# Kernel tuning notes

Hardware: AMD Instinct MI355X
Metric: run time of the kernel (lower is better)

## Reference

```python
import jax, jax.numpy as jnp
import numpy as np

N_NODES = 50000
N_EDGES = 800000
NFEAT = 128
NHID = 64
NLAYER = 3
BN_EPS = 1e-5


def _bn(h, gamma, beta):
    # BatchNorm1d, training-mode batch statistics (biased variance)
    mu = jnp.mean(h, axis=0)
    var = jnp.mean((h - mu) ** 2, axis=0)
    return gamma * (h - mu) * jax.lax.rsqrt(var + BN_EPS) + beta


def setup_inputs() -> dict:
    key = jax.random.key(0)
    ks = jax.random.split(key, 8)
    x = jax.random.normal(ks[0], (N_NODES, NFEAT), dtype=jnp.float32)
    edge_index = jax.random.randint(ks[1], (2, N_EDGES), 0, N_NODES, dtype=jnp.int64)
    # transform: Linear(nfeat, nhid) with bias, then BN
    W_t = jax.random.normal(ks[2], (NFEAT, NHID), dtype=jnp.float32) / np.sqrt(NFEAT)
    b_t = jnp.zeros((NHID,), dtype=jnp.float32)
    g_t = jnp.ones((NHID,), dtype=jnp.float32)
    bb_t = jnp.zeros((NHID,), dtype=jnp.float32)
    # per-layer GIN MLPs (bias=False) and BN affine params, stacked over layers
    W1 = jax.random.normal(ks[3], (NLAYER, NHID, NHID), dtype=jnp.float32) / np.sqrt(NHID)
    W2 = jax.random.normal(ks[4], (NLAYER, NHID, NHID), dtype=jnp.float32) / np.sqrt(NHID)
    gamma = jnp.ones((NLAYER, NHID), dtype=jnp.float32)
    beta = jnp.zeros((NLAYER, NHID), dtype=jnp.float32)
    return {"x": x, "edge_index": edge_index, "W_t": W_t, "b_t": b_t,
            "g_t": g_t, "bb_t": bb_t, "W1": W1, "W2": W2,
            "gamma": gamma, "beta": beta}


def reference(x, edge_index, W_t, b_t, g_t, bb_t, W1, W2, gamma, beta):
    src, dst = edge_index[0], edge_index[1]
    # input transform: Linear + BN
    h = _bn(x @ W_t + b_t, g_t, bb_t)
    for i in range(NLAYER):
        # dropout p=0 -> identity
        # GINConv (eps=0): (1+eps)*h + sum_{j->i} h_j, then 2-layer MLP
        agg = h + jax.ops.segment_sum(h[src], dst, num_segments=N_NODES)
        h = jax.nn.relu(agg @ W1[i]) @ W2[i]
        h = jax.nn.relu(h)
        h = _bn(h, gamma[i], beta[i])
    # per-graph boolean-mask split is a pure partition of rows; return full matrix
    return h
```

## Files before the change

kernel.cpp:

```cpp
#include <hip/hip_runtime.h>

#define NND 50000
#define NED 800000
#define NF  128
#define NH  64
#define BN_EPS 1e-5
#define NCOPY 64
#define SCB  256
#define NSB  ((NND + SCB - 1) / SCB)
#define XNODES (NND / 8)
#define FCH  196

#define WS_HA     0
#define WS_STATS  12800000
#define WS_SSF    (WS_STATS + NCOPY*128*8)
#define WS_DEG    (WS_SSF + 512)
#define WS_OFFS   (WS_DEG + NND*4)
#define WS_CUR    (WS_OFFS + (NND+4)*4)
#define WS_PARTS  (WS_CUR + NND*4)
#define WS_ESRC   (WS_PARTS + 256*4)

__global__ __launch_bounds__(256) void k_deg(const int* __restrict__ dst,
                                             int* __restrict__ deg) {
    int xcd = blockIdx.x & 7;
    int chunk = blockIdx.x >> 3;
    int lo = xcd * XNODES;
    const int4* d4 = (const int4*)dst;
#pragma unroll
    for (int r = 0; r < 4; ++r) {
        int i = chunk * 1024 + r * 256 + threadIdx.x;
        if (i < NED / 4) {
            int4 d = d4[i];
            if ((unsigned)(d.x - lo) < XNODES) atomicAdd(&deg[d.x], 1);
            if ((unsigned)(d.y - lo) < XNODES) atomicAdd(&deg[d.y], 1);
            if ((unsigned)(d.z - lo) < XNODES) atomicAdd(&deg[d.z], 1);
            if ((unsigned)(d.w - lo) < XNODES) atomicAdd(&deg[d.w], 1);
        }
    }
}

__global__ __launch_bounds__(256) void k_fill(const int* __restrict__ src,
                                              const int* __restrict__ dst,
                                              int* __restrict__ cur,
                                              int* __restrict__ esrc) {
    int xcd = blockIdx.x & 7;
    int chunk = blockIdx.x >> 3;
    int lo = xcd * XNODES;
    const int4* d4 = (const int4*)dst;
#pragma unroll
    for (int r = 0; r < 4; ++r) {
        int i = chunk * 1024 + r * 256 + threadIdx.x;
        if (i < NED / 4) {
            int4 d = d4[i];
            int e = i * 4;
            if ((unsigned)(d.x - lo) < XNODES) esrc[atomicAdd(&cur[d.x], 1)] = src[e];
            if ((unsigned)(d.y - lo) < XNODES) esrc[atomicAdd(&cur[d.y], 1)] = src[e + 1];
            if ((unsigned)(d.z - lo) < XNODES) esrc[atomicAdd(&cur[d.z], 1)] = src[e + 2];
            if ((unsigned)(d.w - lo) < XNODES) esrc[atomicAdd(&cur[d.w], 1)] = src[e + 3];
        }
    }
}

__global__ __launch_bounds__(SCB) void k_part(const int* __restrict__ deg,
                                              int* __restrict__ offs,
                                              int* __restrict__ parts) {
    __shared__ int sd[SCB];
    int t = threadIdx.x;
    int i = blockIdx.x * SCB + t;
    int v = (i < NND) ? deg[i] : 0;
    sd[t] = v;
    __syncthreads();
#pragma unroll
    for (int off = 1; off < SCB; off <<= 1) {
        int u = (t >= off) ? sd[t - off] : 0;
        __syncthreads();
        sd[t] += u;
        __syncthreads();
    }
    if (i < NND) offs[i] = sd[t] - v;
    if (t == SCB - 1) parts[blockIdx.x] = sd[t];
}

__global__ __launch_bounds__(256) void k_scan2(int* __restrict__ parts) {
    __shared__ int sd[256];
    int t = threadIdx.x;
    int v = (t < NSB) ? parts[t] : 0;
    sd[t] = v;
    __syncthreads();
#pragma unroll
    for (int off = 1; off < 256; off <<= 1) {
        int u = (t >= off) ? sd[t - off] : 0;
        __syncthreads();
        sd[t] += u;
        __syncthreads();
    }
    if (t < NSB) parts[t] = sd[t] - v;
}

__global__ __launch_bounds__(256) void k_apply(int* __restrict__ offs,
                                               const int* __restrict__ parts,
                                               int* __restrict__ cur) {
    int i = blockIdx.x * 256 + threadIdx.x;
    if (i < NND) {
        int o = offs[i] + parts[i >> 8];
        offs[i] = o;
        cur[i] = o;
    }
    if (i == NND) offs[NND] = NED;
}

__global__ void k_fin(double* __restrict__ st,
                      const float* __restrict__ g, const float* __restrict__ b,
                      float* __restrict__ ssout) {
    int c = threadIdx.x;
    double sum = 0.0, ssq = 0.0;
    for (int cp = 0; cp < NCOPY; ++cp) {
        sum += st[cp * 128 + c];
        ssq += st[cp * 128 + 64 + c];
    }
    for (int cp = 0; cp < NCOPY; ++cp) {
        st[cp * 128 + c] = 0.0;
        st[cp * 128 + 64 + c] = 0.0;
    }
    double mu  = sum / (double)NND;
    double var = ssq / (double)NND - mu * mu;
    if (var < 0.0) var = 0.0;
    double rs = 1.0 / sqrt(var + BN_EPS);
    double sc = (double)g[c] * rs;
    ssout[c]      = (float)sc;
    ssout[64 + c] = (float)((double)b[c] - mu * sc);
}

__global__ __launch_bounds__(128) void k_transform(const float* __restrict__ x,
                                                   const float* __restrict__ Wt,
                                                   const float* __restrict__ bt,
                                                   float* __restrict__ outraw,
                                                   double* __restrict__ stats) {
    __shared__ __align__(16) float Wl[NF * NH];
    __shared__ __align__(16) float sTbuf[2 * 64 * 68];
    int tid  = threadIdx.x;
    int wave = tid >> 6, lane = tid & 63;
    int ti = lane & 7, tj = lane >> 3;
    int tile = blockIdx.x * 2 + wave;
    int base = tile * 64;
    float* sTw = &sTbuf[wave * 64 * 68];
    const float4* x4 = (const float4*)x;

#pragma unroll
    for (int r = 0; r < 16; ++r) {
        int i4 = r * 128 + tid;
        ((float4*)Wl)[i4] = ((const float4*)Wt)[i4];
    }

    float acc[8][8];
#pragma unroll
    for (int i = 0; i < 8; ++i)
#pragma unroll
        for (int j = 0; j < 8; ++j) acc[i][j] = 0.f;

    for (int ch = 0; ch < 2; ++ch) {
        __syncthreads();
#pragma unroll
        for (int s = 0; s < 16; ++s) {
            int flat = s * 64 + lane;
            int nl = flat >> 4, q = flat & 15;
            float4 v = {0.f, 0.f, 0.f, 0.f};
            if (base + nl < NND) v = x4[(size_t)(base + nl) * 32 + ch * 16 + q];
            sTw[(q * 4 + 0) * 68 + nl] = v.x;
            sTw[(q * 4 + 1) * 68 + nl] = v.y;
            sTw[(q * 4 + 2) * 68 + nl] = v.z;
            sTw[(q * 4 + 3) * 68 + nl] = v.w;
        }
        __syncthreads();
#pragma unroll 2
        for (int k = 0; k < 64; ++k) {
            const float* ap = &sTw[k * 68 + ti * 8];
            float4 alo = *(const float4*)ap;
            float4 ahi = *(const float4*)(ap + 4);
            const float* wp = &Wl[(ch * 64 + k) * NH + tj * 8];
            float4 wlo = *(const float4*)wp;
            float4 whi = *(const float4*)(wp + 4);
            float a8[8] = {alo.x, alo.y, alo.z, alo.w, ahi.x, ahi.y, ahi.z, ahi.w};
            float w8[8] = {wlo.x, wlo.y, wlo.z, wlo.w, whi.x, whi.y, whi.z, whi.w};
#pragma unroll
            for (int i = 0; i < 8; ++i)
#pragma unroll
                for (int j = 0; j < 8; ++j) acc[i][j] += a8[i] * w8[j];
        }
    }

    float b8[8];
    *(float4*)&b8[0] = ((const float4*)bt)[tj * 2];
    *(float4*)&b8[4] = ((const float4*)bt)[tj * 2 + 1];

    float s8[8], q8[8];
#pragma unroll
    for (int j = 0; j < 8; ++j) { s8[j] = 0.f; q8[j] = 0.f; }
#pragma unroll
    for (int i = 0; i < 8; ++i) {
        int n = base + ti * 8 + i;
        if (n < NND) {
            float o[8];
#pragma unroll
            for (int j = 0; j < 8; ++j) {
                o[j] = acc[i][j] + b8[j];
                s8[j] += o[j];
                q8[j] += o[j] * o[j];
            }
            *(float4*)&outraw[(size_t)n * NH + tj * 8]     = *(float4*)&o[0];
            *(float4*)&outraw[(size_t)n * NH + tj * 8 + 4] = *(float4*)&o[4];
        }
    }
#pragma unroll
    for (int m = 1; m < 8; m <<= 1) {
#pragma unroll
        for (int j = 0; j < 8; ++j) {
            s8[j] += __shfl_xor(s8[j], m);
            q8[j] += __shfl_xor(q8[j], m);
        }
    }
    if (ti == 0) {
        int slot = (tile & (NCOPY - 1)) * 128 + tj * 8;
#pragma unroll
        for (int j = 0; j < 8; ++j) {
            atomicAdd(&stats[slot + j], (double)s8[j]);
            atomicAdd(&stats[slot + 64 + j], (double)q8[j]);
        }
    }
}

__global__ __launch_bounds__(256) void k_agg(const float* __restrict__ inraw,
                                             float* __restrict__ aggout,
                                             const float* __restrict__ ss,
                                             const int* __restrict__ offs,
                                             const int* __restrict__ esrc) {
    int tid  = threadIdx.x;
    int lane = tid & 63;
    int wv   = tid >> 6;
    int n = blockIdx.x * 4 + wv;
    int q = lane & 15;
    int r = lane >> 4;
    const float4* in4 = (const float4*)inraw;

    int e0 = offs[n], e1 = offs[n + 1];
    int deg = e1 - e0;

    float4 self = make_float4(0.f, 0.f, 0.f, 0.f);
    if (r == 0) self = in4[(size_t)n * 16 + q];

    float ax = 0.f, ay = 0.f, az = 0.f, aw = 0.f;
    for (int bb = e0; bb < e1; bb += 64) {
        int m = e1 - bb; if (m > 64) m = 64;
        int idx = (lane < m) ? esrc[bb + lane] : 0;
        int t = 0;
        for (; t + 16 <= m; t += 16) {
            int j0 = __shfl(idx, t + r);
            int j1 = __shfl(idx, t + 4 + r);
            int j2 = __shfl(idx, t + 8 + r);
            int j3 = __shfl(idx, t + 12 + r);
            float4 v0 = in4[(size_t)j0 * 16 + q];
            float4 v1 = in4[(size_t)j1 * 16 + q];
            float4 v2 = in4[(size_t)j2 * 16 + q];
            float4 v3 = in4[(size_t)j3 * 16 + q];
            ax += (v0.x + v1.x) + (v2.x + v3.x);
            ay += (v0.y + v1.y) + (v2.y + v3.y);
            az += (v0.z + v1.z) + (v2.z + v3.z);
            aw += (v0.w + v1.w) + (v2.w + v3.w);
        }
        for (; t < m; t += 4) {
            int e = t + r;
            int j = __shfl(idx, e & 63);
            if (e < m) {
                float4 v = in4[(size_t)j * 16 + q];
                ax += v.x; ay += v.y; az += v.z; aw += v.w;
            }
        }
    }

    ax += __shfl_xor(ax, 16); ay += __shfl_xor(ay, 16);
    az += __shfl_xor(az, 16); aw += __shfl_xor(aw, 16);
    ax += __shfl_xor(ax, 32); ay += __shfl_xor(ay, 32);
    az += __shfl_xor(az, 32); aw += __shfl_xor(aw, 32);

    if (r == 0) {
        float4 sc4 = ((const float4*)ss)[q];
        float4 sh4 = ((const float4*)(ss + 64))[q];
        float dn = (float)(deg + 1);
        float4 res;
        res.x = sc4.x * (ax + self.x) + dn * sh4.x;
        res.y = sc4.y * (ay + self.y) + dn * sh4.y;
        res.z = sc4.z * (az + self.z) + dn * sh4.z;
        res.w = sc4.w * (aw + self.w) + dn * sh4.w;
        ((float4*)aggout)[(size_t)n * 16 + q] = res;
    }
}

__global__ __launch_bounds__(128) void k_mlp(float* __restrict__ h,
                                             double* __restrict__ statsout,
                                             const float* __restrict__ W1,
                                             const float* __restrict__ W2) {
    __shared__ __align__(16) float W1l[NH * NH];
    __shared__ __align__(16) float W2l[NH * NH];
    __shared__ __align__(16) float sTbuf[2 * 64 * 68];
    int tid  = threadIdx.x;
    int wave = tid >> 6, lane = tid & 63;
    int ti = lane & 7, tj = lane >> 3;
    int tile = blockIdx.x * 2 + wave;
    int base = tile * 64;
    float* sTw = &sTbuf[wave * 64 * 68];
    const float4* h4 = (const float4*)h;

#pragma unroll
    for (int r = 0; r < 8; ++r) {
        int i4 = r * 128 + tid;
        ((float4*)W1l)[i4] = ((const float4*)W1)[i4];
        ((float4*)W2l)[i4] = ((const float4*)W2)[i4];
    }
#pragma unroll
    for (int s = 0; s < 16; ++s) {
        int flat = s * 64 + lane;
        int nl = flat >> 4, q = flat & 15;
        float4 v = {0.f, 0.f, 0.f, 0.f};
        if (base + nl < NND) v = h4[(size_t)(base + nl) * 16 + q];
        sTw[(q * 4 + 0) * 68 + nl] = v.x;
        sTw[(q * 4 + 1) * 68 + nl] = v.y;
        sTw[(q * 4 + 2) * 68 + nl] = v.z;
        sTw[(q * 4 + 3) * 68 + nl] = v.w;
    }
    __syncthreads();

    float acc[8][8];
#pragma unroll
    for (int i = 0; i < 8; ++i)
#pragma unroll
        for (int j = 0; j < 8; ++j) acc[i][j] = 0.f;
#pragma unroll 2
    for (int k = 0; k < 64; ++k) {
        const float* ap = &sTw[k * 68 + ti * 8];
        float4 alo = *(const float4*)ap;
        float4 ahi = *(const float4*)(ap + 4);
        const float* wp = &W1l[k * NH + tj * 8];
        float4 wlo = *(const float4*)wp;
        float4 whi = *(const float4*)(wp + 4);
        float a8[8] = {alo.x, alo.y, alo.z, alo.w, ahi.x, ahi.y, ahi.z, ahi.w};
        float w8[8] = {wlo.x, wlo.y, wlo.z, wlo.w, whi.x, whi.y, whi.z, whi.w};
#pragma unroll
        for (int i = 0; i < 8; ++i)
#pragma unroll
            for (int j = 0; j < 8; ++j) acc[i][j] += a8[i] * w8[j];
    }
#pragma unroll
    for (int i = 0; i < 8; ++i)
#pragma unroll
        for (int j = 0; j < 8; ++j) acc[i][j] = fmaxf(acc[i][j], 0.f);

    __syncthreads();
#pragma unroll
    for (int j = 0; j < 8; ++j) {
        float* p = &sTw[(tj * 8 + j) * 68 + ti * 8];
        float4 lo = {acc[0][j], acc[1][j], acc[2][j], acc[3][j]};
        float4 hi = {acc[4][j], acc[5][j], acc[6][j], acc[7][j]};
        *(float4*)p = lo;
        *(float4*)(p + 4) = hi;
    }
    __syncthreads();

    float a2[8][8];
#pragma unroll
    for (int i = 0; i < 8; ++i)
#pragma unroll
        for (int j = 0; j < 8; ++j) a2[i][j] = 0.f;
#pragma unroll 2
    for (int k = 0; k < 64; ++k) {
        const float* ap = &sTw[k * 68 + ti * 8];
        float4 alo = *(const float4*)ap;
        float4 ahi = *(const float4*)(ap + 4);
        const float* wp = &W2l[k * NH + tj * 8];
        float4 wlo = *(const float4*)wp;
        float4 whi = *(const float4*)(wp + 4);
        float a8[8] = {alo.x, alo.y, alo.z, alo.w, ahi.x, ahi.y, ahi.z, ahi.w};
        float w8[8] = {wlo.x, wlo.y, wlo.z, wlo.w, whi.x, whi.y, whi.z, whi.w};
#pragma unroll
        for (int i = 0; i < 8; ++i)
#pragma unroll
            for (int j = 0; j < 8; ++j) a2[i][j] += a8[i] * w8[j];
    }

    float s8[8], q8[8];
#pragma unroll
    for (int j = 0; j < 8; ++j) { s8[j] = 0.f; q8[j] = 0.f; }
#pragma unroll
    for (int i = 0; i < 8; ++i) {
        int n = base + ti * 8 + i;
        if (n < NND) {
            float o[8];
#pragma unroll
            for (int j = 0; j < 8; ++j) {
                o[j] = fmaxf(a2[i][j], 0.f);
                s8[j] += o[j];
                q8[j] += o[j] * o[j];
            }
            *(float4*)&h[(size_t)n * NH + tj * 8]     = *(float4*)&o[0];
            *(float4*)&h[(size_t)n * NH + tj * 8 + 4] = *(float4*)&o[4];
        }
    }
#pragma unroll
    for (int m = 1; m < 8; m <<= 1) {
#pragma unroll
        for (int j = 0; j < 8; ++j) {
            s8[j] += __shfl_xor(s8[j], m);
            q8[j] += __shfl_xor(q8[j], m);
        }
    }
    if (ti == 0) {
        int slot = (tile & (NCOPY - 1)) * 128 + tj * 8;
#pragma unroll
        for (int j = 0; j < 8; ++j) {
            atomicAdd(&statsout[slot + j], (double)s8[j]);
            atomicAdd(&statsout[slot + 64 + j], (double)q8[j]);
        }
    }
}

__global__ void k_bnout(float* __restrict__ h, const float* __restrict__ ss) {
    int i4 = blockIdx.x * 256 + threadIdx.x;
    if (i4 < NND * NH / 4) {
        int cg = i4 & 15;
        float4 v   = ((float4*)h)[i4];
        float4 scv = ((const float4*)ss)[cg];
        float4 shv = ((const float4*)(ss + 64))[cg];
        v.x = v.x * scv.x + shv.x;
        v.y = v.y * scv.y + shv.y;
        v.z = v.z * scv.z + shv.z;
        v.w = v.w * scv.w + shv.w;
        ((float4*)h)[i4] = v;
    }
}

extern "C" void kernel_launch(void* const* d_in, const int* in_sizes, int n_in,
                              void* d_out, int out_size, void* d_ws, size_t ws_size,
                              hipStream_t stream) {
    const float* x     = (const float*)d_in[0];
    const int*   ei    = (const int*)d_in[1];
    const float* Wt    = (const float*)d_in[2];
    const float* bt    = (const float*)d_in[3];
    const float* gt    = (const float*)d_in[4];
    const float* bbt   = (const float*)d_in[5];
    const float* W1    = (const float*)d_in[6];
    const float* W2    = (const float*)d_in[7];
    const float* gamma = (const float*)d_in[8];
    const float* beta  = (const float*)d_in[9];
    float* out = (float*)d_out;

    char* ws = (char*)d_ws;
    float*  hA    = (float*)(ws + WS_HA);
    double* stats = (double*)(ws + WS_STATS);
    float*  ssf   = (float*)(ws + WS_SSF);
    int*    deg   = (int*)(ws + WS_DEG);
    int*    offs  = (int*)(ws + WS_OFFS);
    int*    cur   = (int*)(ws + WS_CUR);
    int*    parts = (int*)(ws + WS_PARTS);
    int*    esrc  = (int*)(ws + WS_ESRC);

    const int* srcv = ei;
    const int* dstv = ei + NED;

    hipMemsetAsync(stats, 0, NCOPY * 128 * 8 + 512 + NND * 4, stream);

    const int PGRID = FCH * 8;
    k_deg<<<PGRID, 256, 0, stream>>>(dstv, deg);
    k_part<<<NSB, SCB, 0, stream>>>(deg, offs, parts);
    k_scan2<<<1, 256, 0, stream>>>(parts);
    k_apply<<<NSB, 256, 0, stream>>>(offs, parts, cur);
    k_fill<<<PGRID, 256, 0, stream>>>(srcv, dstv, cur, esrc);

    const int NT2 = 391;
    const int NB  = NND / 4;

    k_transform<<<NT2, 128, 0, stream>>>(x, Wt, bt, hA, stats);
    k_fin<<<1, 64, 0, stream>>>(stats, gt, bbt, ssf);

    k_agg<<<NB, 256, 0, stream>>>(hA, out, ssf, offs, esrc);
    k_mlp<<<NT2, 128, 0, stream>>>(out, stats, W1, W2);
    k_fin<<<1, 64, 0, stream>>>(stats, gamma, beta, ssf);

    k_agg<<<NB, 256, 0, stream>>>(out, hA, ssf, offs, esrc);
    k_mlp<<<NT2, 128, 0, stream>>>(hA, stats, W1 + 4096, W2 + 4096);
    k_fin<<<1, 64, 0, stream>>>(stats, gamma + 64, beta + 64, ssf);

    k_agg<<<NB, 256, 0, stream>>>(hA, out, ssf, offs, esrc);
    k_mlp<<<NT2, 128, 0, stream>>>(out, stats, W1 + 8192, W2 + 8192);
    k_fin<<<1, 64, 0, stream>>>(stats, gamma + 128, beta + 128, ssf);

    k_bnout<<<(NND * NH / 4 + 255) / 256, 256, 0, stream>>>(out, ssf);
}
```

Baseline: 321.4 us.

## Store intermediate node features in bf16 to halve gather traffic

Hidden features and aggregation outputs are now stored as packed bf16 (round-to-nearest-even) in workspace buffers, and the gather/aggregate kernel reads 16-byte chunks of 8 bf16 values and accumulates in fp32. The MLP kernel unpacks bf16 into shared memory and writes either a bf16 buffer for the next layer or fp32 for the final output. The aim is to halve the memory bytes moved by the random-access neighbor gather and the intermediate writes. The cost is reduced precision in intermediate activations, which may affect accuracy tolerance.

```diff
diff --git a/kernel.cpp b/kernel.cpp
--- a/kernel.cpp
+++ b/kernel.cpp
@@ -11,7 +11,8 @@
 #define XNODES (NND / 8)
 #define FCH  196
 
-#define WS_HA     0
+#define WS_HB     0
+#define WS_AGG    6400000
 #define WS_STATS  12800000
 #define WS_SSF    (WS_STATS + NCOPY*128*8)
 #define WS_DEG    (WS_SSF + 512)
@@ -19,6 +20,20 @@
 #define WS_CUR    (WS_OFFS + (NND+4)*4)
 #define WS_PARTS  (WS_CUR + NND*4)
 #define WS_ESRC   (WS_PARTS + 256*4)
+
+__device__ __forceinline__ unsigned bfrn(float x) {
+    unsigned u = __float_as_uint(x);
+    return (u + 0x7fffu + ((u >> 16) & 1u)) >> 16;
+}
+__device__ __forceinline__ unsigned pk(float lo, float hi) {
+    return bfrn(lo) | (bfrn(hi) << 16);
+}
+__device__ __forceinline__ void upadd(unsigned u, float& lo, float& hi) {
+    lo += __uint_as_float(u << 16);
+    hi += __uint_as_float(u & 0xffff0000u);
+}
+__device__ __forceinline__ float ulo(unsigned u) { return __uint_as_float(u << 16); }
+__device__ __forceinline__ float uhi(unsigned u) { return __uint_as_float(u & 0xffff0000u); }
 
 __global__ __launch_bounds__(256) void k_deg(const int* __restrict__ dst,
                                              int* __restrict__ deg) {
@@ -114,10 +129,12 @@
                       float* __restrict__ ssout) {
     int c = threadIdx.x;
     double sum = 0.0, ssq = 0.0;
+#pragma unroll
     for (int cp = 0; cp < NCOPY; ++cp) {
         sum += st[cp * 128 + c];
         ssq += st[cp * 128 + 64 + c];
     }
+#pragma unroll
     for (int cp = 0; cp < NCOPY; ++cp) {
         st[cp * 128 + c] = 0.0;
         st[cp * 128 + 64 + c] = 0.0;
@@ -134,7 +151,7 @@
 __global__ __launch_bounds__(128) void k_transform(const float* __restrict__ x,
                                                    const float* __restrict__ Wt,
                                                    const float* __restrict__ bt,
-                                                   float* __restrict__ outraw,
+                                                   uint4* __restrict__ hB4,
                                                    double* __restrict__ stats) {
     __shared__ __align__(16) float Wl[NF * NH];
     __shared__ __align__(16) float sTbuf[2 * 64 * 68];
@@ -207,8 +224,10 @@
                 s8[j] += o[j];
                 q8[j] += o[j] * o[j];
             }
-            *(float4*)&outraw[(size_t)n * NH + tj * 8]     = *(float4*)&o[0];
-            *(float4*)&outraw[(size_t)n * NH + tj * 8 + 4] = *(float4*)&o[4];
+            uint4 ov;
+            ov.x = pk(o[0], o[1]); ov.y = pk(o[2], o[3]);
+            ov.z = pk(o[4], o[5]); ov.w = pk(o[6], o[7]);
+            hB4[(size_t)n * 8 + tj] = ov;
         }
     }
 #pragma unroll
@@ -229,8 +248,8 @@
     }
 }
 
-__global__ __launch_bounds__(256) void k_agg(const float* __restrict__ inraw,
-                                             float* __restrict__ aggout,
+__global__ __launch_bounds__(256) void k_agg(const uint4* __restrict__ hB4,
+                                             uint4* __restrict__ aggB4,
                                              const float* __restrict__ ss,
                                              const int* __restrict__ offs,
                                              const int* __restrict__ esrc) {
@@ -238,64 +257,83 @@
     int lane = tid & 63;
     int wv   = tid >> 6;
     int n = blockIdx.x * 4 + wv;
-    int q = lane & 15;
-    int r = lane >> 4;
-    const float4* in4 = (const float4*)inraw;
+    int q = lane & 7;
+    int r = lane >> 3;
 
     int e0 = offs[n], e1 = offs[n + 1];
     int deg = e1 - e0;
 
-    float4 self = make_float4(0.f, 0.f, 0.f, 0.f);
-    if (r == 0) self = in4[(size_t)n * 16 + q];
-
-    float ax = 0.f, ay = 0.f, az = 0.f, aw = 0.f;
+    float a[8];
+#pragma unroll
+    for (int i = 0; i < 8; ++i) a[i] = 0.f;
+
+    if (r == 0) {
+        uint4 u = hB4[(size_t)n * 8 + q];
+        upadd(u.x, a[0], a[1]); upadd(u.y, a[2], a[3]);
+        upadd(u.z, a[4], a[5]); upadd(u.w, a[6], a[7]);
+    }
+
     for (int bb = e0; bb < e1; bb += 64) {
         int m = e1 - bb; if (m > 64) m = 64;
         int idx = (lane < m) ? esrc[bb + lane] : 0;
         int t = 0;
-        for (; t + 16 <= m; t += 16) {
+        for (; t + 32 <= m; t += 32) {
             int j0 = __shfl(idx, t + r);
-            int j1 = __shfl(idx, t + 4 + r);
-            int j2 = __shfl(idx, t + 8 + r);
-            int j3 = __shfl(idx, t + 12 + r);
-            float4 v0 = in4[(size_t)j0 * 16 + q];
-            float4 v1 = in4[(size_t)j1 * 16 + q];
-            float4 v2 = in4[(size_t)j2 * 16 + q];
-            float4 v3 = in4[(size_t)j3 * 16 + q];
-            ax += (v0.x + v1.x) + (v2.x + v3.x);
-            ay += (v0.y + v1.y) + (v2.y + v3.y);
-            az += (v0.z + v1.z) + (v2.z + v3.z);
-            aw += (v0.w + v1.w) + (v2.w + v3.w);
-        }
-        for (; t < m; t += 4) {
+            int j1 = __shfl(idx, t + 8 + r);
+            int j2 = __shfl(idx, t + 16 + r);
+            int j3 = __shfl(idx, t + 24 + r);
+            uint4 u0 = hB4[(size_t)j0 * 8 + q];
+            uint4 u1 = hB4[(size_t)j1 * 8 + q];
+            uint4 u2 = hB4[(size_t)j2 * 8 + q];
+            uint4 u3 = hB4[(size_t)j3 * 8 + q];
+            upadd(u0.x, a[0], a[1]); upadd(u0.y, a[2], a[3]);
+            upadd(u0.z, a[4], a[5]); upadd(u0.w, a[6], a[7]);
+            upadd(u1.x, a[0], a[1]); upadd(u1.y, a[2], a[3]);
+            upadd(u1.z, a[4], a[5]); upadd(u1.w, a[6], a[7]);
+            upadd(u2.x, a[0], a[1]); upadd(u2.y, a[2], a[3]);
+            upadd(u2.z, a[4], a[5]); upadd(u2.w, a[6], a[7]);
+            upadd(u3.x, a[0], a[1]); upadd(u3.y, a[2], a[3]);
+            upadd(u3.z, a[4], a[5]); upadd(u3.w, a[6], a[7]);
+        }
+        for (; t < m; t += 8) {
             int e = t + r;
             int j = __shfl(idx, e & 63);
             if (e < m) {
-                float4 v = in4[(size_t)j * 16 + q];
-                ax += v.x; ay += v.y; az += v.z; aw += v.w;
+                uint4 u = hB4[(size_t)j * 8 + q];
+                upadd(u.x, a[0], a[1]); upadd(u.y, a[2], a[3]);
+                upadd(u.z, a[4], a[5]); upadd(u.w, a[6], a[7]);
             }
         }
     }
 
-    ax += __shfl_xor(ax, 16); ay += __shfl_xor(ay, 16);
-    az += __shfl_xor(az, 16); aw += __shfl_xor(aw, 16);
-    ax += __shfl_xor(ax, 32); ay += __shfl_xor(ay, 32);
-    az += __shfl_xor(az, 32); aw += __shfl_xor(aw, 32);
+#pragma unroll
+    for (int msk = 8; msk <= 32; msk <<= 1)
+#pragma unroll
+        for (int i = 0; i < 8; ++i) a[i] += __shfl_xor(a[i], msk);
 
     if (r == 0) {
-        float4 sc4 = ((const float4*)ss)[q];
-        float4 sh4 = ((const float4*)(ss + 64))[q];
+        float4 scA = ((const float4*)ss)[q * 2];
+        float4 scB = ((const float4*)ss)[q * 2 + 1];
+        float4 shA = ((const float4*)(ss + 64))[q * 2];
+        float4 shB = ((const float4*)(ss + 64))[q * 2 + 1];
         float dn = (float)(deg + 1);
-        float4 res;
-        res.x = sc4.x * (ax + self.x) + dn * sh4.x;
-        res.y = sc4.y * (ay + self.y) + dn * sh4.y;
-        res.z = sc4.z * (az + self.z) + dn * sh4.z;
-        res.w = sc4.w * (aw + self.w) + dn * sh4.w;
-        ((float4*)aggout)[(size_t)n * 16 + q] = res;
-    }
-}
-
-__global__ __launch_bounds__(128) void k_mlp(float* __restrict__ h,
+        float r0 = scA.x * a[0] + dn * shA.x;
+        float r1 = scA.y * a[1] + dn * shA.y;
+        float r2 = scA.z * a[2] + dn * shA.z;
+        float r3 = scA.w * a[3] + dn * shA.w;
+        float r4 = scB.x * a[4] + dn * shB.x;
+        float r5 = scB.y * a[5] + dn * shB.y;
+        float r6 = scB.z * a[6] + dn * shB.z;
+        float r7 = scB.w * a[7] + dn * shB.w;
+        uint4 ov;
+        ov.x = pk(r0, r1); ov.y = pk(r2, r3); ov.z = pk(r4, r5); ov.w = pk(r6, r7);
+        aggB4[(size_t)n * 8 + q] = ov;
+    }
+}
+
+__global__ __launch_bounds__(128) void k_mlp(const uint4* __restrict__ aggB4,
+                                             float* __restrict__ outF,
+                                             uint4* __restrict__ hBo,
                                              double* __restrict__ statsout,
                                              const float* __restrict__ W1,
                                              const float* __restrict__ W2) {
@@ -308,7 +346,6 @@
     int tile = blockIdx.x * 2 + wave;
     int base = tile * 64;
     float* sTw = &sTbuf[wave * 64 * 68];
-    const float4* h4 = (const float4*)h;
 
 #pragma unroll
     for (int r = 0; r < 8; ++r) {
@@ -317,15 +354,19 @@
         ((float4*)W2l)[i4] = ((const float4*)W2)[i4];
     }
 #pragma unroll
-    for (int s = 0; s < 16; ++s) {
-        int flat = s * 64 + lane;
-        int nl = flat >> 4, q = flat & 15;
-        float4 v = {0.f, 0.f, 0.f, 0.f};
-        if (base + nl < NND) v = h4[(size_t)(base + nl) * 16 + q];
-        sTw[(q * 4 + 0) * 68 + nl] = v.x;
-        sTw[(q * 4 + 1) * 68 + nl] = v.y;
-        sTw[(q * 4 + 2) * 68 + nl] = v.z;
-        sTw[(q * 4 + 3) * 68 + nl] = v.w;
+    for (int s = 0; s < 8; ++s) {
+        int i4 = s * 64 + lane;
+        int nl = i4 >> 3, q = i4 & 7;
+        uint4 u = make_uint4(0u, 0u, 0u, 0u);
+        if (base + nl < NND) u = aggB4[(size_t)(base + nl) * 8 + q];
+        sTw[(q * 8 + 0) * 68 + nl] = ulo(u.x);
+        sTw[(q * 8 + 1) * 68 + nl] = uhi(u.x);
+        sTw[(q * 8 + 2) * 68 + nl] = ulo(u.y);
+        sTw[(q * 8 + 3) * 68 + nl] = uhi(u.y);
+        sTw[(q * 8 + 4) * 68 + nl] = ulo(u.z);
+        sTw[(q * 8 + 5) * 68 + nl] = uhi(u.z);
+        sTw[(q * 8 + 6) * 68 + nl] = ulo(u.w);
+        sTw[(q * 8 + 7) * 68 + nl] = uhi(u.w);
     }
     __syncthreads();
 
@@ -400,8 +441,16 @@
                 s8[j] += o[j];
                 q8[j] += o[j] * o[j];
             }
-            *(float4*)&h[(size_t)n * NH + tj * 8]     = *(float4*)&o[0];
-            *(float4*)&h[(size_t)n * NH + tj * 8 + 4] = *(float4*)&o[4];
+            if (outF) {
+                *(float4*)&outF[(size_t)n * NH + tj * 8]     = *(float4*)&o[0];
+                *(float4*)&outF[(size_t)n * NH + tj * 8 + 4] = *(float4*)&o[4];
+            }
+            if (hBo) {
+                uint4 ov;
+                ov.x = pk(o[0], o[1]); ov.y = pk(o[2], o[3]);
+                ov.z = pk(o[4], o[5]); ov.w = pk(o[6], o[7]);
+                hBo[(size_t)n * 8 + tj] = ov;
+            }
         }
     }
 #pragma unroll
@@ -453,7 +502,8 @@
     float* out = (float*)d_out;
 
     char* ws = (char*)d_ws;
-    float*  hA    = (float*)(ws + WS_HA);
+    uint4*  hB    = (uint4*)(ws + WS_HB);
+    uint4*  aggB  = (uint4*)(ws + WS_AGG);
     double* stats = (double*)(ws + WS_STATS);
     float*  ssf   = (float*)(ws + WS_SSF);
     int*    deg   = (int*)(ws + WS_DEG);
@@ -477,19 +527,19 @@
     const int NT2 = 391;
     const int NB  = NND / 4;
 
-    k_transform<<<NT2, 128, 0, stream>>>(x, Wt, bt, hA, stats);
+    k_transform<<<NT2, 128, 0, stream>>>(x, Wt, bt, hB, stats);
     k_fin<<<1, 64, 0, stream>>>(stats, gt, bbt, ssf);
 
-    k_agg<<<NB, 256, 0, stream>>>(hA, out, ssf, offs, esrc);
-    k_mlp<<<NT2, 128, 0, stream>>>(out, stats, W1, W2);
+    k_agg<<<NB, 256, 0, stream>>>(hB, aggB, ssf, offs, esrc);
+    k_mlp<<<NT2, 128, 0, stream>>>(aggB, nullptr, hB, stats, W1, W2);
     k_fin<<<1, 64, 0, stream>>>(stats, gamma, beta, ssf);
 
-    k_agg<<<NB, 256, 0, stream>>>(out, hA, ssf, offs, esrc);
-    k_mlp<<<NT2, 128, 0, stream>>>(hA, stats, W1 + 4096, W2 + 4096);
+    k_agg<<<NB, 256, 0, stream>>>(hB, aggB, ssf, offs, esrc);
+    k_mlp<<<NT2, 128, 0, stream>>>(aggB, nullptr, hB, stats, W1 + 4096, W2 + 4096);
     k_fin<<<1, 64, 0, stream>>>(stats, gamma + 64, beta + 64, ssf);
 
-    k_agg<<<NB, 256, 0, stream>>>(hA, out, ssf, offs, esrc);
-    k_mlp<<<NT2, 128, 0, stream>>>(out, stats, W1 + 8192, W2 + 8192);
+    k_agg<<<NB, 256, 0, stream>>>(hB, aggB, ssf, offs, esrc);
+    k_mlp<<<NT2, 128, 0, stream>>>(aggB, out, nullptr, stats, W1 + 8192, W2 + 8192);
     k_fin<<<1, 64, 0, stream>>>(stats, gamma + 128, beta + 128, ssf);
 
     k_bnout<<<(NND * NH / 4 + 255) / 256, 256, 0, stream>>>(out, ssf);
```

After: 405.8 us. 1.26x slower.
